# Kernel tuning notes

Hardware: AMD Instinct MI355X
Metric: run time of the kernel (lower is better)

The kernel has to match this reference:

```python
import jax, jax.numpy as jnp
import numpy as np

B = 16384      # batch of Monte Carlo paths
N = 100        # time steps
DIM_W = 3
DT = 0.01
SQRT_DT = DT ** 0.5
SIGMA0 = 0.5   # constant diffusion coefficient (concrete sigma = SIGMA0 * ones(B,1,DIM_W))


def _mlp(x, W1, b1, W2, b2, W3, b3):
    h = jax.nn.relu(x @ W1 + b1)
    h = jax.nn.relu(h @ W2 + b2)
    return h @ W3 + b3


def setup_inputs() -> dict:
    key = jax.random.key(0)
    ks = jax.random.split(key, 8)
    s = 0.1  # modest weight scale for numerical sanity
    return {
        'y0': jnp.ones((1,), jnp.float32),
        'Y0': jnp.zeros((1, 1), jnp.float32),
        'zW1': s * jax.random.normal(ks[0], (2, 64), jnp.float32),
        'zb1': jnp.zeros((64,), jnp.float32),
        'zW2': s * jax.random.normal(ks[1], (64, 64), jnp.float32),
        'zb2': jnp.zeros((64,), jnp.float32),
        'zW3': s * jax.random.normal(ks[2], (64, 3), jnp.float32),
        'zb3': jnp.zeros((3,), jnp.float32),
        'qW1': s * jax.random.normal(ks[3], (2, 64), jnp.float32),
        'qb1': jnp.zeros((64,), jnp.float32),
        'qW2': s * jax.random.normal(ks[4], (64, 64), jnp.float32),
        'qb2': jnp.zeros((64,), jnp.float32),
        'qW3': s * jax.random.normal(ks[5], (64, 1), jnp.float32),
        'qb3': jnp.zeros((1,), jnp.float32),
        'dW': jax.random.normal(ks[6], (N, B, DIM_W), jnp.float32),
        'dZ': jax.random.normal(ks[7], (N, B, DIM_W), jnp.float32),
    }


def reference(y0, Y0, zW1, zb1, zW2, zb2, zW3, zb3,
              qW1, qb1, qW2, qb2, qW3, qb3, dW, dZ):
    y = jnp.broadcast_to(y0.reshape(1, 1), (B, 1))          # (B,1) state
    Y = jnp.broadcast_to(Y0, (B, 1))                         # (B,1) value process
    t = jnp.zeros((B, 1), jnp.float32)

    def step(carry, noise):
        y, Y, t, loss_acc = carry
        dWi, dZi = noise
        inp = jnp.concatenate([t, y], axis=1)                # (B,2)
        z = _mlp(inp, zW1, zb1, zW2, zb2, zW3, zb3)          # (B,3)
        q = _mlp(inp, qW1, qb1, qW2, qb2, qW3, qb3)          # (B,1)
        f = 0.5 * q * q                                      # generator (B,1)
        dw = dWi * SQRT_DT
        dz = dZi * SQRT_DT
        # sigma = SIGMA0 * ones(B,1,DIM_W); bmm(sigma, dw) = SIGMA0 * sum_j dw_j
        diffusion = SIGMA0 * jnp.sum(dw, axis=1, keepdims=True)
        y_new = y + q * DT + diffusion                       # mu = q
        Y_next = Y - f * DT + jnp.sum(z * dw, axis=1, keepdims=True)
        residual = Y_next - (Y - f * DT + jnp.sum(z * dz, axis=1, keepdims=True))
        loss_acc = loss_acc + jnp.mean(residual * residual)
        return (y_new, Y_next, t + DT, loss_acc), None

    (y, Y, t, total_residual_loss), _ = jax.lax.scan(
        step, (y, Y, t, jnp.float32(0.0)), (dW, dZ))
    terminal = y * y                                         # terminal_cost(y)
    terminal_loss = jnp.mean((Y - terminal) ** 2)
    return terminal_loss + total_residual_loss
```

## Files before the change

### kernel.cpp

```cpp
#include <hip/hip_runtime.h>
#include <hip/hip_bf16.h>

#define BATCH   16384
#define NSTEPS  100
#define DT_     0.01f
#define SQRTDT  0.1f
#define SIGMA0_ 0.5f

typedef _Float16  f16x2  __attribute__((ext_vector_type(2)));
typedef _Float16  f16x4  __attribute__((ext_vector_type(4)));
typedef _Float16  f16x8  __attribute__((ext_vector_type(8)));
typedef __fp16    h16x2  __attribute__((ext_vector_type(2)));
typedef float     f32x4  __attribute__((ext_vector_type(4)));

typedef const __attribute__((address_space(1))) void* gas_ptr;
typedef __attribute__((address_space(3))) void*       las_ptr;

__global__ void zero_out_kernel(float* out) { if (threadIdx.x == 0) out[0] = 0.0f; }

static __device__ __forceinline__ f16x4 pk4(const f32x4& d) {
    union { h16x2 h[2]; f16x4 v; } c;
    c.h[0] = __builtin_amdgcn_cvt_pkrtz(d[0], d[1]);
    c.h[1] = __builtin_amdgcn_cvt_pkrtz(d[2], d[3]);
    return c.v;
}

__launch_bounds__(256, 1)
__global__ void deepbsde_kernel(
    const float* __restrict__ y0,  const float* __restrict__ Y0,
    const float* __restrict__ zW1, const float* __restrict__ zb1,
    const float* __restrict__ zW2, const float* __restrict__ zb2,
    const float* __restrict__ zW3, const float* __restrict__ zb3,
    const float* __restrict__ qW1, const float* __restrict__ qb1,
    const float* __restrict__ qW2, const float* __restrict__ qb2,
    const float* __restrict__ qW3, const float* __restrict__ qb3,
    const float* __restrict__ dW,  const float* __restrict__ dZ,
    float* __restrict__ out)
{
    __shared__ __align__(16) char ring[4][8][384];

    const int tid  = threadIdx.x;
    const int lane = tid & 63;
    const int w    = tid >> 6;
    const int ln15 = lane & 15, q4 = lane >> 4;
    const int gw   = (blockIdx.x << 2) + w;
    const int pbase = gw << 4;

    f16x2 A1z[8], B1z[8], C1z[8], A1q[8], B1q[8], C1q[8];
#pragma unroll
    for (int m = 0; m < 8; ++m) {
        int i0 = 2*m, i1 = 2*m + 1;
        int k0 = 32*(i0 >> 3) + 8*q4 + (i0 & 7);
        int k1 = 32*(i1 >> 3) + 8*q4 + (i1 & 7);
        A1z[m] = (f16x2){(_Float16)zW1[k0],      (_Float16)zW1[k1]};
        B1z[m] = (f16x2){(_Float16)zW1[64 + k0], (_Float16)zW1[64 + k1]};
        C1z[m] = (f16x2){(_Float16)zb1[k0],      (_Float16)zb1[k1]};
        A1q[m] = (f16x2){(_Float16)qW1[k0],      (_Float16)qW1[k1]};
        B1q[m] = (f16x2){(_Float16)qW1[64 + k0], (_Float16)qW1[64 + k1]};
        C1q[m] = (f16x2){(_Float16)qb1[k0],      (_Float16)qb1[k1]};
    }

    f16x8 AfZ[4][2], AfQ[4][2];
#pragma unroll
    for (int tN = 0; tN < 4; ++tN)
#pragma unroll
        for (int f = 0; f < 2; ++f)
#pragma unroll
            for (int j = 0; j < 8; ++j) {
                int k = 32*f + 8*q4 + j, n = 16*tN + ln15;
                AfZ[tN][f][j] = (_Float16)zW2[k*64 + n];
                AfQ[tN][f][j] = (_Float16)qW2[k*64 + n];
            }

    f32x4 b2zv[4], b2qv[4];
#pragma unroll
    for (int tN = 0; tN < 4; ++tN)
#pragma unroll
        for (int r = 0; r < 4; ++r) {
            b2zv[tN][r] = zb2[16*tN + 4*q4 + r];
            b2qv[tN][r] = qb2[16*tN + 4*q4 + r];
        }

    const int c3 = ln15 & 3;
    f16x8 A3[4];
#pragma unroll
    for (int f = 0; f < 4; ++f)
#pragma unroll
        for (int j = 0; j < 8; ++j) {
            int tN = 2*(f & 1) + (j >> 2);
            int n  = 16*tN + 4*q4 + (j & 3);
            float wv = (f < 2) ? ((c3 < 3)  ? SQRTDT * zW3[n*3 + c3] : 0.0f)
                               : ((c3 == 3) ? qW3[n]                 : 0.0f);
            A3[f][j] = (_Float16)wv;
        }

    float y = y0[0], Yv = Y0[0], t = 0.0f, acc = 0.0f;
    const float zb30s = SQRTDT * zb3[0], zb31s = SQRTDT * zb3[1],
                zb32s = SQRTDT * zb3[2], qb30  = qb3[0];
    const float CSIG = SIGMA0_ * SQRTDT;
    const float NHDT = -0.5f * DT_;

    const f16x2 zero2h = {(_Float16)0.0f, (_Float16)0.0f};
    const f16x4 zero4h = {(_Float16)0.0f, (_Float16)0.0f, (_Float16)0.0f, (_Float16)0.0f};
    const f32x4 zero4  = {0.0f, 0.0f, 0.0f, 0.0f};

    auto fill = [&](int i) {
        if (lane < 24) {
            const char* g = (lane < 12)
                ? (const char*)dW + ((size_t)i * BATCH + pbase) * 12 + (size_t)lane * 16
                : (const char*)dZ + ((size_t)i * BATCH + pbase) * 12 + (size_t)(lane - 12) * 16;
            __builtin_amdgcn_global_load_lds((gas_ptr)g, (las_ptr)&ring[w][i & 7][0],
                                             16, 0, 0);
        }
    };
    fill(0); fill(1); fill(2); fill(3);

    auto body = [&](int i) {
        const float* sl = (const float*)&ring[w][i & 7][0];
        float nw0 = sl[ln15*3 + 0], nw1 = sl[ln15*3 + 1], nw2 = sl[ln15*3 + 2];
        float nz0 = sl[48 + ln15*3 + 0], nz1 = sl[48 + ln15*3 + 1], nz2 = sl[48 + ln15*3 + 2];

        _Float16 th = (_Float16)t, yh = (_Float16)y;
        const f16x2 tv = {th, th}, yv = {yh, yh};
        union { f16x2 h[4]; f16x8 v; } bz0, bz1, bq0, bq1;
#pragma unroll
        for (int m = 0; m < 8; ++m) {
            f16x2 hz = __builtin_elementwise_max((f16x2)(B1z[m]*yv + (A1z[m]*tv + C1z[m])), zero2h);
            f16x2 hq = __builtin_elementwise_max((f16x2)(B1q[m]*yv + (A1q[m]*tv + C1q[m])), zero2h);
            if (m < 4) { bz0.h[m] = hz;     bq0.h[m] = hq; }
            else       { bz1.h[m - 4] = hz; bq1.h[m - 4] = hq; }
        }

        union { f16x4 q[4]; f16x8 o[2]; } Bz, Bq;
#pragma unroll
        for (int tN = 0; tN < 4; ++tN) {
            f32x4 dz = b2zv[tN];
            dz = __builtin_amdgcn_mfma_f32_16x16x32_f16(AfZ[tN][0], bz0.v, dz, 0, 0, 0);
            dz = __builtin_amdgcn_mfma_f32_16x16x32_f16(AfZ[tN][1], bz1.v, dz, 0, 0, 0);
            f32x4 dq = b2qv[tN];
            dq = __builtin_amdgcn_mfma_f32_16x16x32_f16(AfQ[tN][0], bq0.v, dq, 0, 0, 0);
            dq = __builtin_amdgcn_mfma_f32_16x16x32_f16(AfQ[tN][1], bq1.v, dq, 0, 0, 0);
            Bz.q[tN] = __builtin_elementwise_max(pk4(dz), zero4h);
            Bq.q[tN] = __builtin_elementwise_max(pk4(dq), zero4h);
        }

        f32x4 Pz = zero4, Pq = zero4;
        Pz = __builtin_amdgcn_mfma_f32_16x16x32_f16(A3[0], Bz.o[0], Pz, 0, 0, 0);
        Pz = __builtin_amdgcn_mfma_f32_16x16x32_f16(A3[1], Bz.o[1], Pz, 0, 0, 0);
        Pq = __builtin_amdgcn_mfma_f32_16x16x32_f16(A3[2], Bq.o[0], Pq, 0, 0, 0);
        Pq = __builtin_amdgcn_mfma_f32_16x16x32_f16(A3[3], Bq.o[1], Pq, 0, 0, 0);
        f32x4 P = Pz + Pq;

        float zs0 = P[0] + zb30s, zs1 = P[1] + zb31s, zs2 = P[2] + zb32s;
        float qv  = P[3] + qb30;

        float zdw = fmaf(zs2, nw2, fmaf(zs1, nw1, zs0*nw0));
        float zdz = fmaf(zs2, nz2, fmaf(zs1, nz1, zs0*nz0));
        float snw = (nw0 + nw1) + nw2;
        Yv = fmaf(NHDT*qv, qv, Yv) + zdw;
        float r = zdw - zdz;
        acc = fmaf(r, r, acc);
        y = fmaf(qv, DT_, y);
        y = fmaf(CSIG, snw, y);
        t += DT_;
    };

#pragma unroll 1
    for (int i = 0; i < NSTEPS - 4; ++i) {
        __builtin_amdgcn_s_waitcnt(0x0F73);
        fill(i + 4);
        body(i);
    }
    __builtin_amdgcn_s_waitcnt(0x0F70);
#pragma unroll 1
    for (int i = NSTEPS - 4; i < NSTEPS; ++i) body(i);

    float dterm = Yv - y*y;
    acc = fmaf(dterm, dterm, acc);

    float val = (q4 == 0) ? acc : 0.0f;
#pragma unroll
    for (int off = 1; off < 64; off <<= 1) val += __shfl_xor(val, off);
    if (lane == 0) atomicAdd(out, val * (1.0f / BATCH));
}

extern "C" void kernel_launch(void* const* d_in, const int* in_sizes, int n_in,
                              void* d_out, int out_size, void* d_ws, size_t ws_size,
                              hipStream_t stream)
{
    zero_out_kernel<<<1, 64, 0, stream>>>((float*)d_out);
    deepbsde_kernel<<<256, 256, 0, stream>>>(
        (const float*)d_in[0],  (const float*)d_in[1],
        (const float*)d_in[2],  (const float*)d_in[3],
        (const float*)d_in[4],  (const float*)d_in[5],
        (const float*)d_in[6],  (const float*)d_in[7],
        (const float*)d_in[8],  (const float*)d_in[9],
        (const float*)d_in[10], (const float*)d_in[11],
        (const float*)d_in[12], (const float*)d_in[13],
        (const float*)d_in[14], (const float*)d_in[15],
        (float*)d_out);
}
```

Measured before the change: 162.7 us.

## Precompute time-dependent first-layer terms in LDS table and double-buffer per step

Builds a shared-memory table of W1_t*t + b1 for every time step before the main loop. Each step then loads the next step's entries from LDS one iteration ahead into ping-pong registers, so the per-step first layer needs only the y FMA. The loop is also unrolled by two, and the layer-3 bias is folded into the MFMA accumulator init. This cuts VALU work and register pressure on the serial critical path, at the cost of a prologue that fills 25 KB of LDS and a block-wide barrier.

```diff
diff --git a/kernel.cpp b/kernel.cpp
--- a/kernel.cpp
+++ b/kernel.cpp
@@ -38,6 +38,7 @@
     float* __restrict__ out)
 {
     __shared__ __align__(16) char ring[4][8][384];
+    __shared__ __align__(16) _Float16 tbl[NSTEPS * 128];
 
     const int tid  = threadIdx.x;
     const int lane = tid & 63;
@@ -45,64 +46,6 @@
     const int ln15 = lane & 15, q4 = lane >> 4;
     const int gw   = (blockIdx.x << 2) + w;
     const int pbase = gw << 4;
-
-    f16x2 A1z[8], B1z[8], C1z[8], A1q[8], B1q[8], C1q[8];
-#pragma unroll
-    for (int m = 0; m < 8; ++m) {
-        int i0 = 2*m, i1 = 2*m + 1;
-        int k0 = 32*(i0 >> 3) + 8*q4 + (i0 & 7);
-        int k1 = 32*(i1 >> 3) + 8*q4 + (i1 & 7);
-        A1z[m] = (f16x2){(_Float16)zW1[k0],      (_Float16)zW1[k1]};
-        B1z[m] = (f16x2){(_Float16)zW1[64 + k0], (_Float16)zW1[64 + k1]};
-        C1z[m] = (f16x2){(_Float16)zb1[k0],      (_Float16)zb1[k1]};
-        A1q[m] = (f16x2){(_Float16)qW1[k0],      (_Float16)qW1[k1]};
-        B1q[m] = (f16x2){(_Float16)qW1[64 + k0], (_Float16)qW1[64 + k1]};
-        C1q[m] = (f16x2){(_Float16)qb1[k0],      (_Float16)qb1[k1]};
-    }
-
-    f16x8 AfZ[4][2], AfQ[4][2];
-#pragma unroll
-    for (int tN = 0; tN < 4; ++tN)
-#pragma unroll
-        for (int f = 0; f < 2; ++f)
-#pragma unroll
-            for (int j = 0; j < 8; ++j) {
-                int k = 32*f + 8*q4 + j, n = 16*tN + ln15;
-                AfZ[tN][f][j] = (_Float16)zW2[k*64 + n];
-                AfQ[tN][f][j] = (_Float16)qW2[k*64 + n];
-            }
-
-    f32x4 b2zv[4], b2qv[4];
-#pragma unroll
-    for (int tN = 0; tN < 4; ++tN)
-#pragma unroll
-        for (int r = 0; r < 4; ++r) {
-            b2zv[tN][r] = zb2[16*tN + 4*q4 + r];
-            b2qv[tN][r] = qb2[16*tN + 4*q4 + r];
-        }
-
-    const int c3 = ln15 & 3;
-    f16x8 A3[4];
-#pragma unroll
-    for (int f = 0; f < 4; ++f)
-#pragma unroll
-        for (int j = 0; j < 8; ++j) {
-            int tN = 2*(f & 1) + (j >> 2);
-            int n  = 16*tN + 4*q4 + (j & 3);
-            float wv = (f < 2) ? ((c3 < 3)  ? SQRTDT * zW3[n*3 + c3] : 0.0f)
-                               : ((c3 == 3) ? qW3[n]                 : 0.0f);
-            A3[f][j] = (_Float16)wv;
-        }
-
-    float y = y0[0], Yv = Y0[0], t = 0.0f, acc = 0.0f;
-    const float zb30s = SQRTDT * zb3[0], zb31s = SQRTDT * zb3[1],
-                zb32s = SQRTDT * zb3[2], qb30  = qb3[0];
-    const float CSIG = SIGMA0_ * SQRTDT;
-    const float NHDT = -0.5f * DT_;
-
-    const f16x2 zero2h = {(_Float16)0.0f, (_Float16)0.0f};
-    const f16x4 zero4h = {(_Float16)0.0f, (_Float16)0.0f, (_Float16)0.0f, (_Float16)0.0f};
-    const f32x4 zero4  = {0.0f, 0.0f, 0.0f, 0.0f};
 
     auto fill = [&](int i) {
         if (lane < 24) {
@@ -115,20 +58,109 @@
     };
     fill(0); fill(1); fill(2); fill(3);
 
-    auto body = [&](int i) {
+    {
+        float tt = 0.0f;
+        for (int i = 0; i < NSTEPS; ++i) {
+            int r = (tid - (i << 6)) & 255;
+            if (r < 64) {
+                int q4e = r >> 4, mlp = (r >> 3) & 1, m = r & 7;
+                const float* Wp = mlp ? qW1 : zW1;
+                const float* bp = mlp ? qb1 : zb1;
+                int i0 = 2*m, i1 = 2*m + 1;
+                int k0 = 32*(i0 >> 3) + 8*q4e + (i0 & 7);
+                int k1 = 32*(i1 >> 3) + 8*q4e + (i1 & 7);
+                _Float16 th = (_Float16)tt;
+                f16x2 A = {(_Float16)Wp[k0], (_Float16)Wp[k1]};
+                f16x2 C = {(_Float16)bp[k0], (_Float16)bp[k1]};
+                f16x2 tv = {th, th};
+                f16x2 v = A*tv + C;
+                int idx = (i*4 + q4e)*16 + mlp*8 + m;
+                *(f16x2*)&tbl[idx << 1] = v;
+            }
+            tt += DT_;
+        }
+    }
+
+    f16x2 B1z[8], B1q[8];
+#pragma unroll
+    for (int m = 0; m < 8; ++m) {
+        int i0 = 2*m, i1 = 2*m + 1;
+        int k0 = 32*(i0 >> 3) + 8*q4 + (i0 & 7);
+        int k1 = 32*(i1 >> 3) + 8*q4 + (i1 & 7);
+        B1z[m] = (f16x2){(_Float16)zW1[64 + k0], (_Float16)zW1[64 + k1]};
+        B1q[m] = (f16x2){(_Float16)qW1[64 + k0], (_Float16)qW1[64 + k1]};
+    }
+
+    f16x8 AfZ[4][2], AfQ[4][2];
+#pragma unroll
+    for (int tN = 0; tN < 4; ++tN)
+#pragma unroll
+        for (int f = 0; f < 2; ++f)
+#pragma unroll
+            for (int j = 0; j < 8; ++j) {
+                int k = 32*f + 8*q4 + j, n = 16*tN + ln15;
+                AfZ[tN][f][j] = (_Float16)zW2[k*64 + n];
+                AfQ[tN][f][j] = (_Float16)qW2[k*64 + n];
+            }
+
+    f32x4 b2zv[4], b2qv[4];
+#pragma unroll
+    for (int tN = 0; tN < 4; ++tN)
+#pragma unroll
+        for (int r = 0; r < 4; ++r) {
+            b2zv[tN][r] = zb2[16*tN + 4*q4 + r];
+            b2qv[tN][r] = qb2[16*tN + 4*q4 + r];
+        }
+
+    const int c3 = ln15 & 3;
+    f16x8 A3[4];
+#pragma unroll
+    for (int f = 0; f < 4; ++f)
+#pragma unroll
+        for (int j = 0; j < 8; ++j) {
+            int tN = 2*(f & 1) + (j >> 2);
+            int n  = 16*tN + 4*q4 + (j & 3);
+            float wv = (f < 2) ? ((c3 < 3)  ? SQRTDT * zW3[n*3 + c3] : 0.0f)
+                               : ((c3 == 3) ? qW3[n]                 : 0.0f);
+            A3[f][j] = (_Float16)wv;
+        }
+
+    float y = y0[0], Yv = Y0[0], acc = 0.0f;
+    const float CSIG = SIGMA0_ * SQRTDT;
+    const float NHDT = -0.5f * DT_;
+    const f32x4 C3bias = {SQRTDT * zb3[0], SQRTDT * zb3[1], SQRTDT * zb3[2], qb3[0]};
+
+    const f16x2 zero2h = {(_Float16)0.0f, (_Float16)0.0f};
+    const f16x4 zero4h = {(_Float16)0.0f, (_Float16)0.0f, (_Float16)0.0f, (_Float16)0.0f};
+    const f32x4 zero4  = {0.0f, 0.0f, 0.0f, 0.0f};
+
+    f16x8 cz0, cz1, cq0, cq1, dz0, dz1, dq0, dq1;
+
+    auto body = [&](int i,
+                    f16x8& tz0, f16x8& tz1, f16x8& tq0, f16x8& tq1,
+                    f16x8& uz0, f16x8& uz1, f16x8& uq0, f16x8& uq1) {
         const float* sl = (const float*)&ring[w][i & 7][0];
         float nw0 = sl[ln15*3 + 0], nw1 = sl[ln15*3 + 1], nw2 = sl[ln15*3 + 2];
         float nz0 = sl[48 + ln15*3 + 0], nz1 = sl[48 + ln15*3 + 1], nz2 = sl[48 + ln15*3 + 2];
 
-        _Float16 th = (_Float16)t, yh = (_Float16)y;
-        const f16x2 tv = {th, th}, yv = {yh, yh};
+        int ip = i + 1; ip = (ip > NSTEPS - 1) ? NSTEPS - 1 : ip;
+        {
+            const f16x8* tp = (const f16x8*)(tbl + (ip*4 + q4)*32);
+            uz0 = tp[0]; uz1 = tp[1]; uq0 = tp[2]; uq1 = tp[3];
+        }
+
+        _Float16 yh = (_Float16)y;
+        const f16x2 yv = {yh, yh};
+        union U8 { f16x8 v; f16x2 h[4]; };
+        U8 Tz0; Tz0.v = tz0; U8 Tz1; Tz1.v = tz1;
+        U8 Tq0; Tq0.v = tq0; U8 Tq1; Tq1.v = tq1;
         union { f16x2 h[4]; f16x8 v; } bz0, bz1, bq0, bq1;
 #pragma unroll
-        for (int m = 0; m < 8; ++m) {
-            f16x2 hz = __builtin_elementwise_max((f16x2)(B1z[m]*yv + (A1z[m]*tv + C1z[m])), zero2h);
-            f16x2 hq = __builtin_elementwise_max((f16x2)(B1q[m]*yv + (A1q[m]*tv + C1q[m])), zero2h);
-            if (m < 4) { bz0.h[m] = hz;     bq0.h[m] = hq; }
-            else       { bz1.h[m - 4] = hz; bq1.h[m - 4] = hq; }
+        for (int m = 0; m < 4; ++m) {
+            bz0.h[m] = __builtin_elementwise_max((f16x2)(B1z[m]*yv + Tz0.h[m]), zero2h);
+            bq0.h[m] = __builtin_elementwise_max((f16x2)(B1q[m]*yv + Tq0.h[m]), zero2h);
+            bz1.h[m] = __builtin_elementwise_max((f16x2)(B1z[m+4]*yv + Tz1.h[m]), zero2h);
+            bq1.h[m] = __builtin_elementwise_max((f16x2)(B1q[m+4]*yv + Tq1.h[m]), zero2h);
         }
 
         union { f16x4 q[4]; f16x8 o[2]; } Bz, Bq;
@@ -144,36 +176,43 @@
             Bq.q[tN] = __builtin_elementwise_max(pk4(dq), zero4h);
         }
 
-        f32x4 Pz = zero4, Pq = zero4;
+        f32x4 Pz = C3bias, Pq = zero4;
         Pz = __builtin_amdgcn_mfma_f32_16x16x32_f16(A3[0], Bz.o[0], Pz, 0, 0, 0);
         Pz = __builtin_amdgcn_mfma_f32_16x16x32_f16(A3[1], Bz.o[1], Pz, 0, 0, 0);
         Pq = __builtin_amdgcn_mfma_f32_16x16x32_f16(A3[2], Bq.o[0], Pq, 0, 0, 0);
         Pq = __builtin_amdgcn_mfma_f32_16x16x32_f16(A3[3], Bq.o[1], Pq, 0, 0, 0);
         f32x4 P = Pz + Pq;
 
-        float zs0 = P[0] + zb30s, zs1 = P[1] + zb31s, zs2 = P[2] + zb32s;
-        float qv  = P[3] + qb30;
-
+        float zs0 = P[0], zs1 = P[1], zs2 = P[2], qv = P[3];
         float zdw = fmaf(zs2, nw2, fmaf(zs1, nw1, zs0*nw0));
         float zdz = fmaf(zs2, nz2, fmaf(zs1, nz1, zs0*nz0));
         float snw = (nw0 + nw1) + nw2;
         Yv = fmaf(NHDT*qv, qv, Yv) + zdw;
         float r = zdw - zdz;
         acc = fmaf(r, r, acc);
-        y = fmaf(qv, DT_, y);
-        y = fmaf(CSIG, snw, y);
-        t += DT_;
+        y = fmaf(CSIG, snw, fmaf(qv, DT_, y));
     };
 
+    __syncthreads();
+    {
+        const f16x8* tp0 = (const f16x8*)(tbl + q4*32);
+        cz0 = tp0[0]; cz1 = tp0[1]; cq0 = tp0[2]; cq1 = tp0[3];
+    }
+
 #pragma unroll 1
-    for (int i = 0; i < NSTEPS - 4; ++i) {
+    for (int i = 0; i < NSTEPS - 4; i += 2) {
         __builtin_amdgcn_s_waitcnt(0x0F73);
         fill(i + 4);
-        body(i);
+        body(i,     cz0, cz1, cq0, cq1, dz0, dz1, dq0, dq1);
+        __builtin_amdgcn_s_waitcnt(0x0F73);
+        fill(i + 5);
+        body(i + 1, dz0, dz1, dq0, dq1, cz0, cz1, cq0, cq1);
     }
     __builtin_amdgcn_s_waitcnt(0x0F70);
-#pragma unroll 1
-    for (int i = NSTEPS - 4; i < NSTEPS; ++i) body(i);
+    body(NSTEPS - 4, cz0, cz1, cq0, cq1, dz0, dz1, dq0, dq1);
+    body(NSTEPS - 3, dz0, dz1, dq0, dq1, cz0, cz1, cq0, cq1);
+    body(NSTEPS - 2, cz0, cz1, cq0, cq1, dz0, dz1, dq0, dq1);
+    body(NSTEPS - 1, dz0, dz1, dq0, dq1, cz0, cz1, cq0, cq1);
 
     float dterm = Yv - y*y;
     acc = fmaf(dterm, dterm, acc);
```

Measured after the change: 164.8 us. Within noise of the previous version (+1.3%).
